# Optimization experiments

Hardware: AMD Instinct MI355X
Metric: run time of the kernel (lower is better)

The kernel has to match this reference:

```python
import jax, jax.numpy as jnp
import numpy as np

TAU = 0.2  # args.gumble_tau


def _segment_softmax(vals, seg, num_seg):
    # torch.sparse.softmax(dim=1): softmax over the nonzero entries of each row
    m = jax.ops.segment_max(vals, seg, num_segments=num_seg)
    e = jnp.exp(vals - m[seg])
    s = jax.ops.segment_sum(e, seg, num_segments=num_seg)
    return e / s[seg]


def _masked_attention(q_embed, k_embed, Wq, bq, Wk, bk, rows, cols, noise, num_rows):
    # Q = self.Q(q_embed); K = self.K(k_embed)
    Q = q_embed @ Wq + bq            # [Nq, H]
    K = k_embed @ Wk + bk            # [Nk, H]
    # sparse_dense_mul(adj, Q @ K.T) -> only gather edge entries (same math)
    w = jnp.sum(Q[rows] * K[cols], axis=-1)   # [E]
    g = jnp.log(-jnp.log(noise))              # gumble_G = log(-log(rand))
    z = (w - g) / TAU
    return _segment_softmax(z, rows, num_rows)


def setup_inputs() -> dict:
    key = jax.random.key(0)
    ks = jax.random.split(key, 10)
    U, I, D, H, E = 50000, 25000, 256, 128, 1600000
    inp = {
        "user_embed": jax.random.normal(ks[0], (U, D), jnp.float32),
        "item_embed": jax.random.normal(ks[1], (I, D), jnp.float32),
        "Wq": jax.random.normal(ks[2], (D, H), jnp.float32) * 0.05,
        "bq": jax.random.normal(ks[3], (H,), jnp.float32) * 0.05,
        "Wk": jax.random.normal(ks[4], (D, H), jnp.float32) * 0.05,
        "bk": jax.random.normal(ks[5], (H,), jnp.float32) * 0.05,
        "ui_rows": jax.random.randint(ks[6], (E,), 0, U, jnp.int32),
        "ui_cols": jax.random.randint(ks[7], (E,), 0, I, jnp.int32),
        "noise_ui": jax.random.uniform(ks[8], (E,), jnp.float32, 1e-6, 1.0),
        "noise_iu": jax.random.uniform(ks[9], (E,), jnp.float32, 1e-6, 1.0),
    }
    return inp


def reference(user_embed, item_embed, Wq, bq, Wk, bk, ui_rows, ui_cols, noise_ui, noise_iu):
    U = user_embed.shape[0]
    I = item_embed.shape[0]
    # M_ui: rows = users, softmax over items per user
    vals_ui = _masked_attention(user_embed, item_embed, Wq, bq, Wk, bk,
                                ui_rows, ui_cols, noise_ui, U)
    # M_iu: transposed adjacency, rows = items, same Q/K layers
    vals_iu = _masked_attention(item_embed, user_embed, Wq, bq, Wk, bk,
                                ui_cols, ui_rows, noise_iu, I)
    # mask values = cat([M_ui.values(), M_iu.values()])
    return jnp.concatenate([vals_ui, vals_iu])
```

## Files before the change

kernel.cpp:

```cpp
#include <hip/hip_runtime.h>
#include <hip/hip_fp16.h>
#include <math.h>

#define TAU_INV 5.0f
#define LOG2E   1.4426950408889634f

typedef _Float16 half2v __attribute__((ext_vector_type(2)));
typedef _Float16 f16x8  __attribute__((ext_vector_type(8)));
typedef float    f32x4  __attribute__((ext_vector_type(4)));
typedef float    fv4    __attribute__((ext_vector_type(4)));

__device__ __forceinline__ float fast_exp2(float x) { return __builtin_amdgcn_exp2f(x); }
__device__ __forceinline__ float fast_log2(float x) { return __builtin_amdgcn_logf(x); }

__device__ __forceinline__ double exp_double(float z) {
    float y = z * LOG2E;
    float n = rintf(y);
    float r = y - n;
    float f = fast_exp2(r);
    long long e = (long long)n + 1023;
    if (e < 1)    e = 1;
    if (e > 2046) e = 2046;
    double scale = __longlong_as_double(e << 52);
    return (double)f * scale;
}

__device__ __forceinline__ float log2_of_double(double v) {
    unsigned long long b = __double_as_longlong(v);
    int ex = (int)((b >> 52) & 0x7FFULL) - 1023;
    double m = __longlong_as_double((b & 0xFFFFFFFFFFFFFULL) | 0x3FF0000000000000ULL);
    return (float)ex + fast_log2((float)m);
}

__global__ __launch_bounds__(256) void convert_w(
    const float* __restrict__ Wq, const float* __restrict__ Wk,
    _Float16* __restrict__ Wt_hi, _Float16* __restrict__ Wt_lo,
    double* __restrict__ seg_sumd, int nseg)
{
    int t = blockIdx.x * 256 + threadIdx.x;
    int n = t >> 8;
    int k = t & 255;
    float x = (n < 128) ? Wq[k * 128 + n] : Wk[k * 128 + (n - 128)];
    _Float16 hi = (_Float16)x;
    _Float16 lo = (_Float16)(x - (float)hi);
    Wt_hi[n * 256 + k] = hi;
    Wt_lo[n * 256 + k] = lo;
    for (int i = t; i < nseg; i += 65536) seg_sumd[i] = 0.0;
}

__global__ __launch_bounds__(512) void gemm_qk_mfma(
    const float* __restrict__ Xu, const float* __restrict__ Xi,
    const _Float16* __restrict__ Wt_hi, const _Float16* __restrict__ Wt_lo,
    const float* __restrict__ bq, const float* __restrict__ bk,
    __half* __restrict__ QK, int U, int I)
{
    __shared__ _Float16 Ah[64][72];
    __shared__ _Float16 Al[64][72];

    const int tid  = threadIdx.x;
    const int row0 = blockIdx.x * 64;
    const int wv   = tid >> 6;
    const int l    = tid & 63;
    const int lr   = l & 15;
    const int kc   = l >> 4;
    const int n0   = wv * 32;
    const int NT   = U + I;

    f32x4 acc[4][2];
#pragma unroll
    for (int i = 0; i < 4; ++i)
#pragma unroll
        for (int j = 0; j < 2; ++j)
            acc[i][j] = (f32x4){0.f, 0.f, 0.f, 0.f};

    const int sr = tid >> 3;
    const int sk = (tid & 7) * 8;
    const float* Xrow = nullptr;
    {
        int gr = row0 + sr;
        if (gr < U)       Xrow = &Xu[(size_t)gr * 256];
        else if (gr < NT) Xrow = &Xi[(size_t)(gr - U) * 256];
    }

    for (int k0 = 0; k0 < 256; k0 += 64) {
        {
            fv4 v0, v1;
            if (Xrow) {
                v0 = __builtin_nontemporal_load((const fv4*)(Xrow + k0 + sk));
                v1 = __builtin_nontemporal_load((const fv4*)(Xrow + k0 + sk + 4));
            } else {
                v0 = v1 = (fv4){0.f, 0.f, 0.f, 0.f};
            }
            float x[8] = {v0.x, v0.y, v0.z, v0.w, v1.x, v1.y, v1.z, v1.w};
            _Float16 hi[8], lo[8];
#pragma unroll
            for (int q = 0; q < 8; ++q) {
                hi[q] = (_Float16)x[q];
                lo[q] = (_Float16)(x[q] - (float)hi[q]);
            }
            *(f16x8*)&Ah[sr][sk] = *(const f16x8*)&hi[0];
            *(f16x8*)&Al[sr][sk] = *(const f16x8*)&lo[0];
        }
        __syncthreads();

#pragma unroll
        for (int kk = 0; kk < 2; ++kk) {
            const int kof = kk * 32 + kc * 8;
            f16x8 ah[4], al[4];
#pragma unroll
            for (int i = 0; i < 4; ++i) {
                ah[i] = *(const f16x8*)&Ah[i * 16 + lr][kof];
                al[i] = *(const f16x8*)&Al[i * 16 + lr][kof];
            }
#pragma unroll
            for (int j = 0; j < 2; ++j) {
                const size_t wo = (size_t)(n0 + j * 16 + lr) * 256 + k0 + kof;
                f16x8 bh = *(const f16x8*)&Wt_hi[wo];
                f16x8 bl = *(const f16x8*)&Wt_lo[wo];
#pragma unroll
                for (int i = 0; i < 4; ++i) {
                    acc[i][j] = __builtin_amdgcn_mfma_f32_16x16x32_f16(ah[i], bh, acc[i][j], 0, 0, 0);
                    acc[i][j] = __builtin_amdgcn_mfma_f32_16x16x32_f16(al[i], bh, acc[i][j], 0, 0, 0);
                    acc[i][j] = __builtin_amdgcn_mfma_f32_16x16x32_f16(ah[i], bl, acc[i][j], 0, 0, 0);
                }
            }
        }
        __syncthreads();
    }

    float bias[2];
#pragma unroll
    for (int j = 0; j < 2; ++j) {
        int col = n0 + j * 16 + lr;
        bias[j] = (col < 128) ? bq[col] : bk[col - 128];
    }
#pragma unroll
    for (int i = 0; i < 4; ++i) {
#pragma unroll
        for (int q = 0; q < 4; ++q) {
            int gr = row0 + i * 16 + kc * 4 + q;
            if (gr < NT) {
#pragma unroll
                for (int j = 0; j < 2; ++j) {
                    int col = n0 + j * 16 + lr;
                    QK[(size_t)gr * 256 + col] = __float2half_rn(acc[i][j][q] + bias[j]);
                }
            }
        }
    }
}

__global__ __launch_bounds__(256) void edge_w_both(
    const __half* __restrict__ QK,
    const int* __restrict__ rows, const int* __restrict__ cols,
    const float* __restrict__ noise_ui, const float* __restrict__ noise_iu,
    float* __restrict__ out, double* __restrict__ seg_sumd, int U, int E)
{
    const int gtid = blockIdx.x * 256 + threadIdx.x;
    const int eid  = gtid >> 3;
    if (eid >= E) return;
    const int hl = threadIdx.x & 7;

    const int r = __builtin_nontemporal_load(&rows[eid]);
    const int c = __builtin_nontemporal_load(&cols[eid]);
    const __half* urow = QK + (size_t)r * 256;
    const __half* irow = QK + (size_t)(U + c) * 256;

    const uint4 qu0 = *(const uint4*)(urow + hl * 16);
    const uint4 qu1 = *(const uint4*)(urow + hl * 16 + 8);
    const uint4 ku0 = *(const uint4*)(urow + 128 + hl * 16);
    const uint4 ku1 = *(const uint4*)(urow + 128 + hl * 16 + 8);
    const uint4 qi0 = *(const uint4*)(irow + hl * 16);
    const uint4 qi1 = *(const uint4*)(irow + hl * 16 + 8);
    const uint4 ki0 = *(const uint4*)(irow + 128 + hl * 16);
    const uint4 ki1 = *(const uint4*)(irow + 128 + hl * 16 + 8);

    float d0 = 0.0f, d1 = 0.0f;
    {
        const half2v* a0 = (const half2v*)&qu0;
        const half2v* b0 = (const half2v*)&ki0;
        const half2v* a1 = (const half2v*)&qi0;
        const half2v* b1 = (const half2v*)&ku0;
#pragma unroll
        for (int t = 0; t < 4; ++t) {
            d0 = __builtin_amdgcn_fdot2(a0[t], b0[t], d0, false);
            d1 = __builtin_amdgcn_fdot2(a1[t], b1[t], d1, false);
        }
        const half2v* a0b = (const half2v*)&qu1;
        const half2v* b0b = (const half2v*)&ki1;
        const half2v* a1b = (const half2v*)&qi1;
        const half2v* b1b = (const half2v*)&ku1;
#pragma unroll
        for (int t = 0; t < 4; ++t) {
            d0 = __builtin_amdgcn_fdot2(a0b[t], b0b[t], d0, false);
            d1 = __builtin_amdgcn_fdot2(a1b[t], b1b[t], d1, false);
        }
    }
    d0 += __shfl_xor(d0, 4);  d1 += __shfl_xor(d1, 4);
    d0 += __shfl_xor(d0, 2);  d1 += __shfl_xor(d1, 2);
    d0 += __shfl_xor(d0, 1);  d1 += __shfl_xor(d1, 1);

    if (hl < 2) {
        const int g  = hl;
        const float d  = g ? d1 : d0;
        const float nz = g ? __builtin_nontemporal_load(&noise_iu[eid])
                           : __builtin_nontemporal_load(&noise_ui[eid]);
        const float zz = (d - __logf(-__logf(nz))) * TAU_INV;
        const int s  = g ? (U + c) : r;
        __builtin_nontemporal_store(zz, &out[(size_t)g * E + eid]);
        atomicAdd(&seg_sumd[s], exp_double(zz));
    }
}

__global__ void edge_norm2v(float* __restrict__ z,
                            const int* __restrict__ rows, const int* __restrict__ cols,
                            const double* __restrict__ seg_sumd, int U, int E)
{
    int p = blockIdx.x * blockDim.x + threadIdx.x;
    int i = p * 2;
    if (i >= 2 * E) return;
    const bool iu  = (i >= E);
    const int base = iu ? (i - E) : i;
    const int off  = iu ? U : 0;
    const int* idx = iu ? cols : rows;
    int2 rc   = *(const int2*)&idx[base];
    float2 zz = *(const float2*)&z[i];
    float l0 = log2_of_double(seg_sumd[off + rc.x]);
    float l1 = log2_of_double(seg_sumd[off + rc.y]);
    float o0 = fast_exp2(zz.x * LOG2E - l0);
    float o1 = fast_exp2(zz.y * LOG2E - l1);
    *(float2*)&z[i] = make_float2(o0, o1);
}

__global__ void edge_norm2(float* __restrict__ z,
                           const int* __restrict__ rows, const int* __restrict__ cols,
                           const double* __restrict__ seg_sumd, int U, int E)
{
    int i = blockIdx.x * blockDim.x + threadIdx.x;
    if (i >= 2 * E) return;
    int s = (i < E) ? rows[i] : (U + cols[i - E]);
    float l = log2_of_double(seg_sumd[s]);
    z[i] = fast_exp2(z[i] * LOG2E - l);
}

extern "C" void kernel_launch(void* const* d_in, const int* in_sizes, int n_in,
                              void* d_out, int out_size, void* d_ws, size_t ws_size,
                              hipStream_t stream)
{
    const float* user_embed = (const float*)d_in[0];
    const float* item_embed = (const float*)d_in[1];
    const float* Wq = (const float*)d_in[2];
    const float* bq = (const float*)d_in[3];
    const float* Wk = (const float*)d_in[4];
    const float* bk = (const float*)d_in[5];
    const int* ui_rows    = (const int*)d_in[6];
    const int* ui_cols    = (const int*)d_in[7];
    const float* noise_ui = (const float*)d_in[8];
    const float* noise_iu = (const float*)d_in[9];

    const int H = in_sizes[3];
    const int D = in_sizes[2] / H;
    const int U = in_sizes[0] / D;
    const int I = in_sizes[1] / D;
    const int E = in_sizes[6];

    const int nseg = U + I;

    char* wsc = (char*)d_ws;
    __half* QK = (__half*)wsc;          wsc += (size_t)nseg * 256 * sizeof(__half);
    double* seg_sumd = (double*)wsc;    wsc += (size_t)nseg * sizeof(double);
    _Float16* Wt_hi = (_Float16*)wsc;   wsc += (size_t)256 * 256 * sizeof(_Float16);
    _Float16* Wt_lo = (_Float16*)wsc;   wsc += (size_t)256 * 256 * sizeof(_Float16);

    float* out = (float*)d_out;

    convert_w<<<256, 256, 0, stream>>>(Wq, Wk, Wt_hi, Wt_lo, seg_sumd, nseg);

    const int gblocks = (nseg + 63) / 64;
    gemm_qk_mfma<<<gblocks, 512, 0, stream>>>(user_embed, item_embed,
                                              Wt_hi, Wt_lo, bq, bk, QK, U, I);

    const int eblocks = (int)(((long long)E * 8 + 255) / 256);
    edge_w_both<<<eblocks, 256, 0, stream>>>(QK, ui_rows, ui_cols,
                                             noise_ui, noise_iu,
                                             out, seg_sumd, U, E);

    if ((E & 1) == 0) {
        const int vblocks = (E + 255) / 256;
        edge_norm2v<<<vblocks, 256, 0, stream>>>(out, ui_rows, ui_cols,
                                                 seg_sumd, U, E);
    } else {
        const int sblocks = (2 * E + 255) / 256;
        edge_norm2<<<sblocks, 256, 0, stream>>>(out, ui_rows, ui_cols,
                                                seg_sumd, U, E);
    }
}
```

Baseline: 430.9 us.

## Fuse all stages into one persistent cooperative kernel with grid syncs

Replaces the four-kernel launch sequence (weight conversion, MFMA GEMM, edge scoring, normalization) with one persistent cooperative kernel that separates the phases with grid.sync(). The GEMM phase takes its 64-row tiles from a dynamic atomic counter, which is reset by a memset before each launch. The aim is to remove kernel launch gaps and tail effects between stages. In exchange, the grid is limited to one occupancy-sized wave, grid-wide barriers cost time, and the fixed block count may give less latency hiding in the edge phases than the original oversubscribed launches.

```diff
diff --git a/kernel.cpp b/kernel.cpp
--- a/kernel.cpp
+++ b/kernel.cpp
@@ -1,9 +1,13 @@
 #include <hip/hip_runtime.h>
+#include <hip/hip_cooperative_groups.h>
 #include <hip/hip_fp16.h>
 #include <math.h>
 
+namespace cg = cooperative_groups;
+
 #define TAU_INV 5.0f
 #define LOG2E   1.4426950408889634f
+#define NTHR    512
 
 typedef _Float16 half2v __attribute__((ext_vector_type(2)));
 typedef _Float16 f16x8  __attribute__((ext_vector_type(8)));
@@ -32,6 +36,225 @@
     return (float)ex + fast_log2((float)m);
 }
 
+__global__ __launch_bounds__(NTHR) void fused_pipeline(
+    const float* __restrict__ Xu, const float* __restrict__ Xi,
+    const float* __restrict__ Wq, const float* __restrict__ bq,
+    const float* __restrict__ Wk, const float* __restrict__ bk,
+    const int* __restrict__ rows, const int* __restrict__ cols,
+    const float* __restrict__ noise_ui, const float* __restrict__ noise_iu,
+    float* __restrict__ out, __half* __restrict__ QK,
+    double* __restrict__ seg_sumd,
+    _Float16* __restrict__ Wt_hi, _Float16* __restrict__ Wt_lo,
+    int* __restrict__ ctrl,
+    int U, int I, int E)
+{
+    cg::grid_group grid = cg::this_grid();
+    const int tid    = threadIdx.x;
+    const int bid    = blockIdx.x;
+    const int stride = gridDim.x * NTHR;
+    const int nseg   = U + I;
+    const int NT     = nseg;
+
+    __shared__ _Float16 Ah[64][72];
+    __shared__ _Float16 Al[64][72];
+    __shared__ int tile_s;
+
+    for (int t = bid * NTHR + tid; t < 65536; t += stride) {
+        int n = t >> 8;
+        int k = t & 255;
+        float x = (n < 128) ? Wq[k * 128 + n] : Wk[k * 128 + (n - 128)];
+        _Float16 hi = (_Float16)x;
+        _Float16 lo = (_Float16)(x - (float)hi);
+        Wt_hi[n * 256 + k] = hi;
+        Wt_lo[n * 256 + k] = lo;
+    }
+    for (int i = bid * NTHR + tid; i < nseg; i += stride) seg_sumd[i] = 0.0;
+    grid.sync();
+
+    {
+        const int l  = tid & 63;
+        const int lr = l & 15;
+        const int kc = l >> 4;
+        const int n0 = (tid >> 6) * 32;
+        const int sr = tid >> 3;
+        const int sk = (tid & 7) * 8;
+        const int ntiles = (nseg + 63) / 64;
+
+        for (;;) {
+            if (tid == 0) tile_s = atomicAdd(&ctrl[0], 1);
+            __syncthreads();
+            const int tile = tile_s;
+            if (tile >= ntiles) break;
+            const int row0 = tile * 64;
+
+            f32x4 acc[4][2];
+#pragma unroll
+            for (int i = 0; i < 4; ++i)
+#pragma unroll
+                for (int j = 0; j < 2; ++j)
+                    acc[i][j] = (f32x4){0.f, 0.f, 0.f, 0.f};
+
+            const float* Xrow = nullptr;
+            {
+                int gr = row0 + sr;
+                if (gr < U)       Xrow = &Xu[(size_t)gr * 256];
+                else if (gr < NT) Xrow = &Xi[(size_t)(gr - U) * 256];
+            }
+
+            for (int k0 = 0; k0 < 256; k0 += 64) {
+                {
+                    fv4 v0, v1;
+                    if (Xrow) {
+                        v0 = __builtin_nontemporal_load((const fv4*)(Xrow + k0 + sk));
+                        v1 = __builtin_nontemporal_load((const fv4*)(Xrow + k0 + sk + 4));
+                    } else {
+                        v0 = v1 = (fv4){0.f, 0.f, 0.f, 0.f};
+                    }
+                    float x[8] = {v0.x, v0.y, v0.z, v0.w, v1.x, v1.y, v1.z, v1.w};
+                    _Float16 hi[8], lo[8];
+#pragma unroll
+                    for (int q = 0; q < 8; ++q) {
+                        hi[q] = (_Float16)x[q];
+                        lo[q] = (_Float16)(x[q] - (float)hi[q]);
+                    }
+                    *(f16x8*)&Ah[sr][sk] = *(const f16x8*)&hi[0];
+                    *(f16x8*)&Al[sr][sk] = *(const f16x8*)&lo[0];
+                }
+                __syncthreads();
+
+#pragma unroll
+                for (int kk = 0; kk < 2; ++kk) {
+                    const int kof = kk * 32 + kc * 8;
+                    f16x8 ah[4], al[4];
+#pragma unroll
+                    for (int i = 0; i < 4; ++i) {
+                        ah[i] = *(const f16x8*)&Ah[i * 16 + lr][kof];
+                        al[i] = *(const f16x8*)&Al[i * 16 + lr][kof];
+                    }
+#pragma unroll
+                    for (int j = 0; j < 2; ++j) {
+                        const size_t wo = (size_t)(n0 + j * 16 + lr) * 256 + k0 + kof;
+                        f16x8 bh = *(const f16x8*)&Wt_hi[wo];
+                        f16x8 bl = *(const f16x8*)&Wt_lo[wo];
+#pragma unroll
+                        for (int i = 0; i < 4; ++i) {
+                            acc[i][j] = __builtin_amdgcn_mfma_f32_16x16x32_f16(ah[i], bh, acc[i][j], 0, 0, 0);
+                            acc[i][j] = __builtin_amdgcn_mfma_f32_16x16x32_f16(al[i], bh, acc[i][j], 0, 0, 0);
+                            acc[i][j] = __builtin_amdgcn_mfma_f32_16x16x32_f16(ah[i], bl, acc[i][j], 0, 0, 0);
+                        }
+                    }
+                }
+                __syncthreads();
+            }
+
+            float bias[2];
+#pragma unroll
+            for (int j = 0; j < 2; ++j) {
+                int col = n0 + j * 16 + lr;
+                bias[j] = (col < 128) ? bq[col] : bk[col - 128];
+            }
+#pragma unroll
+            for (int i = 0; i < 4; ++i) {
+#pragma unroll
+                for (int q = 0; q < 4; ++q) {
+                    int gr = row0 + i * 16 + kc * 4 + q;
+                    if (gr < NT) {
+#pragma unroll
+                        for (int j = 0; j < 2; ++j) {
+                            int col = n0 + j * 16 + lr;
+                            QK[(size_t)gr * 256 + col] = __float2half_rn(acc[i][j][q] + bias[j]);
+                        }
+                    }
+                }
+            }
+            __syncthreads();
+        }
+    }
+    grid.sync();
+
+    {
+        const int hl = tid & 7;
+        const long long total = (long long)E * 8;
+        for (long long gt = (long long)bid * NTHR + tid; gt < total; gt += stride) {
+            const int eid = (int)(gt >> 3);
+
+            const int r = __builtin_nontemporal_load(&rows[eid]);
+            const int c = __builtin_nontemporal_load(&cols[eid]);
+            const __half* urow = QK + (size_t)r * 256;
+            const __half* irow = QK + (size_t)(U + c) * 256;
+
+            const uint4 qu0 = *(const uint4*)(urow + hl * 16);
+            const uint4 qu1 = *(const uint4*)(urow + hl * 16 + 8);
+            const uint4 ku0 = *(const uint4*)(urow + 128 + hl * 16);
+            const uint4 ku1 = *(const uint4*)(urow + 128 + hl * 16 + 8);
+            const uint4 qi0 = *(const uint4*)(irow + hl * 16);
+            const uint4 qi1 = *(const uint4*)(irow + hl * 16 + 8);
+            const uint4 ki0 = *(const uint4*)(irow + 128 + hl * 16);
+            const uint4 ki1 = *(const uint4*)(irow + 128 + hl * 16 + 8);
+
+            float d0 = 0.0f, d1 = 0.0f;
+            {
+                const half2v* a0 = (const half2v*)&qu0;
+                const half2v* b0 = (const half2v*)&ki0;
+                const half2v* a1 = (const half2v*)&qi0;
+                const half2v* b1 = (const half2v*)&ku0;
+#pragma unroll
+                for (int t = 0; t < 4; ++t) {
+                    d0 = __builtin_amdgcn_fdot2(a0[t], b0[t], d0, false);
+                    d1 = __builtin_amdgcn_fdot2(a1[t], b1[t], d1, false);
+                }
+                const half2v* a0b = (const half2v*)&qu1;
+                const half2v* b0b = (const half2v*)&ki1;
+                const half2v* a1b = (const half2v*)&qi1;
+                const half2v* b1b = (const half2v*)&ku1;
+#pragma unroll
+                for (int t = 0; t < 4; ++t) {
+                    d0 = __builtin_amdgcn_fdot2(a0b[t], b0b[t], d0, false);
+                    d1 = __builtin_amdgcn_fdot2(a1b[t], b1b[t], d1, false);
+                }
+            }
+            d0 += __shfl_xor(d0, 4);  d1 += __shfl_xor(d1, 4);
+            d0 += __shfl_xor(d0, 2);  d1 += __shfl_xor(d1, 2);
+            d0 += __shfl_xor(d0, 1);  d1 += __shfl_xor(d1, 1);
+
+            if (hl < 2) {
+                const int g  = hl;
+                const float d  = g ? d1 : d0;
+                const float nz = g ? __builtin_nontemporal_load(&noise_iu[eid])
+                                   : __builtin_nontemporal_load(&noise_ui[eid]);
+                const float zz = (d - __logf(-__logf(nz))) * TAU_INV;
+                const int s  = g ? (U + c) : r;
+                __builtin_nontemporal_store(zz, &out[(size_t)g * E + eid]);
+                atomicAdd(&seg_sumd[s], exp_double(zz));
+            }
+        }
+    }
+    grid.sync();
+
+    if ((E & 1) == 0) {
+        for (int p = bid * NTHR + tid; p < E; p += stride) {
+            int i = p * 2;
+            const bool iu  = (i >= E);
+            const int base = iu ? (i - E) : i;
+            const int off  = iu ? U : 0;
+            const int* idx = iu ? cols : rows;
+            int2 rc   = *(const int2*)&idx[base];
+            float2 zz = *(const float2*)&out[i];
+            float l0 = log2_of_double(seg_sumd[off + rc.x]);
+            float l1 = log2_of_double(seg_sumd[off + rc.y]);
+            float o0 = fast_exp2(zz.x * LOG2E - l0);
+            float o1 = fast_exp2(zz.y * LOG2E - l1);
+            *(float2*)&out[i] = make_float2(o0, o1);
+        }
+    } else {
+        for (int i = bid * NTHR + tid; i < 2 * E; i += stride) {
+            int s = (i < E) ? rows[i] : (U + cols[i - E]);
+            float l = log2_of_double(seg_sumd[s]);
+            out[i] = fast_exp2(out[i] * LOG2E - l);
+        }
+    }
+}
+
 __global__ __launch_bounds__(256) void convert_w(
     const float* __restrict__ Wq, const float* __restrict__ Wk,
     _Float16* __restrict__ Wt_hi, _Float16* __restrict__ Wt_lo,
@@ -59,11 +282,10 @@
 
     const int tid  = threadIdx.x;
     const int row0 = blockIdx.x * 64;
-    const int wv   = tid >> 6;
     const int l    = tid & 63;
     const int lr   = l & 15;
     const int kc   = l >> 4;
-    const int n0   = wv * 32;
+    const int n0   = (tid >> 6) * 32;
     const int NT   = U + I;
 
     f32x4 acc[4][2];
@@ -260,9 +482,9 @@
 
     const int H = in_sizes[3];
     const int D = in_sizes[2] / H;
-    const int U = in_sizes[0] / D;
-    const int I = in_sizes[1] / D;
-    const int E = in_sizes[6];
+    int U = in_sizes[0] / D;
+    int I = in_sizes[1] / D;
+    int E = in_sizes[6];
 
     const int nseg = U + I;
 
@@ -271,27 +493,58 @@
     double* seg_sumd = (double*)wsc;    wsc += (size_t)nseg * sizeof(double);
     _Float16* Wt_hi = (_Float16*)wsc;   wsc += (size_t)256 * 256 * sizeof(_Float16);
     _Float16* Wt_lo = (_Float16*)wsc;   wsc += (size_t)256 * 256 * sizeof(_Float16);
+    int* ctrl = (int*)wsc;              wsc += 4 * sizeof(int);
 
     float* out = (float*)d_out;
 
-    convert_w<<<256, 256, 0, stream>>>(Wq, Wk, Wt_hi, Wt_lo, seg_sumd, nseg);
-
-    const int gblocks = (nseg + 63) / 64;
-    gemm_qk_mfma<<<gblocks, 512, 0, stream>>>(user_embed, item_embed,
-                                              Wt_hi, Wt_lo, bq, bk, QK, U, I);
-
-    const int eblocks = (int)(((long long)E * 8 + 255) / 256);
-    edge_w_both<<<eblocks, 256, 0, stream>>>(QK, ui_rows, ui_cols,
-                                             noise_ui, noise_iu,
-                                             out, seg_sumd, U, E);
-
-    if ((E & 1) == 0) {
-        const int vblocks = (E + 255) / 256;
-        edge_norm2v<<<vblocks, 256, 0, stream>>>(out, ui_rows, ui_cols,
-                                                 seg_sumd, U, E);
-    } else {
-        const int sblocks = (2 * E + 255) / 256;
-        edge_norm2<<<sblocks, 256, 0, stream>>>(out, ui_rows, ui_cols,
-                                                seg_sumd, U, E);
-    }
-}
+    static int s_nblk = 0;
+    if (s_nblk == 0) {
+        int dev = 0;
+        (void)hipGetDevice(&dev);
+        int ncu = 256;
+        (void)hipDeviceGetAttribute(&ncu, hipDeviceAttributeMultiprocessorCount, dev);
+        int perCU = 0;
+        if (hipOccupancyMaxActiveBlocksPerMultiprocessor(&perCU, fused_pipeline, NTHR, 0)
+                != hipSuccess || perCU < 1)
+            perCU = 1;
+        s_nblk = ncu * perCU;
+    }
+
+    (void)hipMemsetAsync(ctrl, 0, 4 * sizeof(int), stream);
+
+    void* kargs[] = {
+        (void*)&user_embed, (void*)&item_embed,
+        (void*)&Wq, (void*)&bq, (void*)&Wk, (void*)&bk,
+        (void*)&ui_rows, (void*)&ui_cols,
+        (void*)&noise_ui, (void*)&noise_iu,
+        (void*)&out, (void*)&QK, (void*)&seg_sumd,
+        (void*)&Wt_hi, (void*)&Wt_lo, (void*)&ctrl,
+        (void*)&U, (void*)&I, (void*)&E
+    };
+
+    hipError_t err = hipLaunchCooperativeKernel(
+        fused_pipeline, dim3(s_nblk), dim3(NTHR), kargs, 0, stream);
+
+    if (err != hipSuccess) {
+        convert_w<<<256, 256, 0, stream>>>(Wq, Wk, Wt_hi, Wt_lo, seg_sumd, nseg);
+
+        const int gblocks = (nseg + 63) / 64;
+        gemm_qk_mfma<<<gblocks, 512, 0, stream>>>(user_embed, item_embed,
+                                                  Wt_hi, Wt_lo, bq, bk, QK, U, I);
+
+        const int eblocks = (int)(((long long)E * 8 + 255) / 256);
+        edge_w_both<<<eblocks, 256, 0, stream>>>(QK, ui_rows, ui_cols,
+                                                 noise_ui, noise_iu,
+                                                 out, seg_sumd, U, E);
+
+        if ((E & 1) == 0) {
+            const int vblocks = (E + 255) / 256;
+            edge_norm2v<<<vblocks, 256, 0, stream>>>(out, ui_rows, ui_cols,
+                                                     seg_sumd, U, E);
+        } else {
+            const int sblocks = (2 * E + 255) / 256;
+            edge_norm2<<<sblocks, 256, 0, stream>>>(out, ui_rows, ui_cols,
+                                                    seg_sumd, U, E);
+        }
+    }
+}
```

Result: slower. 560.3 us (+30.0%).
